# Performance work log

Measured on AMD Instinct MI355X. Metric: run time of the kernel, lower is better.

The kernel has to match this reference:

```python
import jax, jax.numpy as jnp
import numpy as np

N_X_AXIS = 128
N_Y_AXIS = 128
X_RANGE = (-2.0, 2.0)
Y_RANGE = (-2.0, 2.0)
BATCH = 4
N_CTX = 1024


def make_grid():
    # Give_2d_Grid: flattened (n_x*n_y, 2) grid, x-major (consistent with
    # the view(batch, n_x_axis, n_y_axis, 3) reshape in forward).
    gx = jnp.linspace(X_RANGE[0], X_RANGE[1], N_X_AXIS, dtype=jnp.float32)
    gy = jnp.linspace(Y_RANGE[0], Y_RANGE[1], N_Y_AXIS, dtype=jnp.float32)
    xx, yy = jnp.meshgrid(gx, gy, indexing='ij')  # (n_x, n_y)
    return jnp.stack([xx.ravel(), yy.ravel()], axis=-1)  # (n_x*n_y, 2)


def setup_inputs() -> dict:
    key = jax.random.key(0)
    k1, k2 = jax.random.split(key)
    X = jax.random.normal(k1, (BATCH, N_CTX, 2), dtype=jnp.float32)
    Y = jax.random.normal(k2, (BATCH, N_CTX, 2), dtype=jnp.float32)
    grid = make_grid()
    return {"X": X, "Y": Y, "grid": grid}


def reference(X, Y, grid):
    # RBF Gram matrix between grid points and context points X.
    # k(a,b) = exp(-||a-b||^2 / (2 l^2)), l = 1 (default length scale).
    # d2: (B, G, n)
    d2 = jnp.sum((grid[None, :, None, :] - X[:, None, :, :]) ** 2, axis=-1)
    Gram = jnp.exp(-0.5 * d2)  # (B, G, n)

    # Psi: prepend a column of ones -> (B, n, 3)
    ones = jnp.ones(Y.shape[:2] + (1,), dtype=Y.dtype)
    Expand_Y = jnp.concatenate([ones, Y], axis=-1)

    # Feature map: (B, G, 3)
    FM = jnp.einsum('bgn,bnc->bgc', Gram, Expand_Y)

    # Density-normalize the value channels by the density channel.
    density = FM[..., 0:1]
    FM = jnp.concatenate([density, FM[..., 1:] / density], axis=-1)

    # (B, G, 3) -> (B, n_x, n_y, 3) -> (B, 3, n_y, n_x)
    out = FM.reshape(X.shape[0], N_X_AXIS, N_Y_AXIS, 3)
    return out.transpose(0, 3, 2, 1)
```

## Files before the change

### kernel.cpp

```cpp
#include <hip/hip_runtime.h>


#define NCTX  1024
#define GPB   16384
#define OUTB  (3 * GPB)

typedef float f32x4  __attribute__((ext_vector_type(4)));
typedef short bf16x8 __attribute__((ext_vector_type(8)));

__device__ __forceinline__ float fast_exp2(float x) {
#if __has_builtin(__builtin_amdgcn_exp2f)
  return __builtin_amdgcn_exp2f(x);
#else
  return exp2f(x);
#endif
}

__device__ __forceinline__ unsigned short f2bf(float f) {
  union { float f; unsigned int u; } v; v.f = f;
  unsigned int r = v.u + 0x7FFFu + ((v.u >> 16) & 1u);
  return (unsigned short)(r >> 16);
}

__global__ __launch_bounds__(256) void tables_kernel(
    const float* __restrict__ X, const float* __restrict__ Y,
    const float* __restrict__ grid,
    unsigned short* __restrict__ A, unsigned short* __restrict__ Bt)
{
  const float SC = 0.84932180028801907f;
  const int blk = blockIdx.x;
  const int t   = threadIdx.x;
  const bool isA = blk < 512;
  const int r   = isA ? blk : blk - 512;
  const int b   = r >> 7;
  const int row = r & 127;
  const float gs = (isA ? grid[2 * row + 1]
                        : grid[2 * (row * 128)])
                   * SC;

  const float2* Xb = (const float2*)(X + b * NCTX * 2);
  const int n0 = 4 * t;

  if (isA) {
    const float2* Yb = (const float2*)(Y + b * NCTX * 2);
    ushort4 o0, o1, o2;
#pragma unroll
    for (int i = 0; i < 4; ++i) {
      float2 x = Xb[n0 + i];
      float2 y = Yb[n0 + i];
      float d  = gs - SC * x.y;
      float e  = fast_exp2(-(d * d));
      ((unsigned short*)&o0)[i] = f2bf(e);
      ((unsigned short*)&o1)[i] = f2bf(e * y.x);
      ((unsigned short*)&o2)[i] = f2bf(e * y.y);
    }
    unsigned short* a0 = A + (size_t)(b * 384 + row) * NCTX + n0;
    *(ushort4*)(a0)                 = o0;
    *(ushort4*)(a0 + 128 * NCTX)    = o1;
    *(ushort4*)(a0 + 256 * NCTX)    = o2;
  } else {
    ushort4 o;
#pragma unroll
    for (int i = 0; i < 4; ++i) {
      float2 x = Xb[n0 + i];
      float d  = gs - SC * x.x;
      ((unsigned short*)&o)[i] = f2bf(fast_exp2(-(d * d)));
    }
    *(ushort4*)(Bt + (size_t)(b * 128 + row) * NCTX + n0) = o;
  }
}

__global__ __launch_bounds__(64) void gemm_kernel(
    const unsigned short* __restrict__ A,
    const unsigned short* __restrict__ Bt,
    float* __restrict__ out)
{
  const int id   = blockIdx.x;
  const int b    = id / 192;
  const int rr   = id % 192;
  const int mt   = rr >> 3;
  const int nt   = rr & 7;
  const int lane = threadIdx.x;
  const int lo   = lane & 15;
  const int quad = lane >> 4;

  const bf16x8* ap = (const bf16x8*)(A  + (size_t)(b * 384 + mt * 16 + lo) * NCTX + quad * 8);
  const bf16x8* bp = (const bf16x8*)(Bt + (size_t)(b * 128 + nt * 16 + lo) * NCTX + quad * 8);

  f32x4 acc = {0.f, 0.f, 0.f, 0.f};
#pragma unroll 8
  for (int s = 0; s < 32; ++s) {
    bf16x8 av = ap[4 * s];
    bf16x8 bv = bp[4 * s];
    acc = __builtin_amdgcn_mfma_f32_16x16x32_bf16(av, bv, acc, 0, 0, 0);
  }

  float* ob = out + (size_t)b * OUTB + nt * 16 + lo;
  const int grow0 = mt * 16 + quad * 4;
#pragma unroll
  for (int g = 0; g < 4; ++g)
    ob[(size_t)(grow0 + g) * 128] = acc[g];
}

__global__ __launch_bounds__(256) void divide_kernel(float* __restrict__ out)
{
  const int id = blockIdx.x * 256 + threadIdx.x;
  const int b  = id >> 13;
  const int r  = id & 8191;
  const int c  = r >> 12;
  const int p4 = r & 4095;
  float4* base = (float4*)(out + (size_t)b * OUTB);
  float4 d = base[p4];
  float4* vp = base + (size_t)(c + 1) * 4096 + p4;
  float4 v = *vp;
  v.x /= d.x; v.y /= d.y; v.z /= d.z; v.w /= d.w;
  *vp = v;
}

extern "C" void kernel_launch(void* const* d_in, const int* in_sizes, int n_in,
                              void* d_out, int out_size, void* d_ws, size_t ws_size,
                              hipStream_t stream) {
  const float* X    = (const float*)d_in[0];
  const float* Y    = (const float*)d_in[1];
  const float* grid = (const float*)d_in[2];
  float* out        = (float*)d_out;

  unsigned short* A  = (unsigned short*)d_ws;
  unsigned short* Bt = A + (size_t)4 * 384 * NCTX;

  tables_kernel<<<dim3(1024), dim3(256), 0, stream>>>(X, Y, grid, A, Bt);
  gemm_kernel  <<<dim3(768),  dim3(64),  0, stream>>>(A, Bt, out);
  divide_kernel<<<dim3(128),  dim3(256), 0, stream>>>(out);
}
```

Measured before the change: 72.39 us.

## Fuse density division into GEMM by computing all three channels per block

The GEMM kernel now computes the density channel and both value channels for the same output tile in one block, reusing the loaded B fragment across three MFMAs. With all three accumulators in registers it divides the value channels by density in the epilogue, which removes the separate divide kernel launch and its global read-modify-write pass. The trade-off is fewer blocks (256 instead of 768) with more work each, which may lower occupancy and latency hiding on a GPU with many CUs.

Measured after the change: 71.58 us. Within noise of the previous version (-1.1%).

```diff
diff --git a/kernel.cpp b/kernel.cpp
--- a/kernel.cpp
+++ b/kernel.cpp
@@ -55,9 +55,9 @@
       ((unsigned short*)&o2)[i] = f2bf(e * y.y);
     }
     unsigned short* a0 = A + (size_t)(b * 384 + row) * NCTX + n0;
-    *(ushort4*)(a0)                 = o0;
-    *(ushort4*)(a0 + 128 * NCTX)    = o1;
-    *(ushort4*)(a0 + 256 * NCTX)    = o2;
+    *(ushort4*)(a0)              = o0;
+    *(ushort4*)(a0 + 128 * NCTX) = o1;
+    *(ushort4*)(a0 + 256 * NCTX) = o2;
   } else {
     ushort4 o;
 #pragma unroll
@@ -70,51 +70,44 @@
   }
 }
 
-__global__ __launch_bounds__(64) void gemm_kernel(
+__global__ __launch_bounds__(64) void gemm_div_kernel(
     const unsigned short* __restrict__ A,
     const unsigned short* __restrict__ Bt,
     float* __restrict__ out)
 {
   const int id   = blockIdx.x;
-  const int b    = id / 192;
-  const int rr   = id % 192;
-  const int mt   = rr >> 3;
-  const int nt   = rr & 7;
+  const int b    = id >> 6;
+  const int jyt  = (id >> 3) & 7;
+  const int ixt  = id & 7;
   const int lane = threadIdx.x;
   const int lo   = lane & 15;
   const int quad = lane >> 4;
 
-  const bf16x8* ap = (const bf16x8*)(A  + (size_t)(b * 384 + mt * 16 + lo) * NCTX + quad * 8);
-  const bf16x8* bp = (const bf16x8*)(Bt + (size_t)(b * 128 + nt * 16 + lo) * NCTX + quad * 8);
+  const size_t koff = (size_t)quad * 8;
+  const unsigned short* a0 = A  + ((size_t)(b * 384) + jyt * 16 + lo) * NCTX + koff;
+  const unsigned short* bp = Bt + ((size_t)(b * 128) + ixt * 16 + lo) * NCTX + koff;
 
-  f32x4 acc = {0.f, 0.f, 0.f, 0.f};
-#pragma unroll 8
+  f32x4 acc0 = {0.f,0.f,0.f,0.f}, acc1 = acc0, acc2 = acc0;
+#pragma unroll 4
   for (int s = 0; s < 32; ++s) {
-    bf16x8 av = ap[4 * s];
-    bf16x8 bv = bp[4 * s];
-    acc = __builtin_amdgcn_mfma_f32_16x16x32_bf16(av, bv, acc, 0, 0, 0);
+    const size_t o = (size_t)s * 32;
+    bf16x8 bv  = *(const bf16x8*)(bp + o);
+    bf16x8 a0v = *(const bf16x8*)(a0 + o);
+    bf16x8 a1v = *(const bf16x8*)(a0 + 128 * NCTX + o);
+    bf16x8 a2v = *(const bf16x8*)(a0 + 256 * NCTX + o);
+    acc0 = __builtin_amdgcn_mfma_f32_16x16x32_bf16(a0v, bv, acc0, 0, 0, 0);
+    acc1 = __builtin_amdgcn_mfma_f32_16x16x32_bf16(a1v, bv, acc1, 0, 0, 0);
+    acc2 = __builtin_amdgcn_mfma_f32_16x16x32_bf16(a2v, bv, acc2, 0, 0, 0);
   }
 
-  float* ob = out + (size_t)b * OUTB + nt * 16 + lo;
-  const int grow0 = mt * 16 + quad * 4;
+  float* ob = out + (size_t)b * OUTB + (jyt * 16 + quad * 4) * 128 + ixt * 16 + lo;
 #pragma unroll
-  for (int g = 0; g < 4; ++g)
-    ob[(size_t)(grow0 + g) * 128] = acc[g];
-}
-
-__global__ __launch_bounds__(256) void divide_kernel(float* __restrict__ out)
-{
-  const int id = blockIdx.x * 256 + threadIdx.x;
-  const int b  = id >> 13;
-  const int r  = id & 8191;
-  const int c  = r >> 12;
-  const int p4 = r & 4095;
-  float4* base = (float4*)(out + (size_t)b * OUTB);
-  float4 d = base[p4];
-  float4* vp = base + (size_t)(c + 1) * 4096 + p4;
-  float4 v = *vp;
-  v.x /= d.x; v.y /= d.y; v.z /= d.z; v.w /= d.w;
-  *vp = v;
+  for (int g = 0; g < 4; ++g) {
+    float d = acc0[g];
+    ob[(size_t)g * 128]               = d;
+    ob[(size_t)g * 128 + GPB]         = acc1[g] / d;
+    ob[(size_t)g * 128 + 2 * GPB]     = acc2[g] / d;
+  }
 }
 
 extern "C" void kernel_launch(void* const* d_in, const int* in_sizes, int n_in,
@@ -128,7 +121,6 @@
   unsigned short* A  = (unsigned short*)d_ws;
   unsigned short* Bt = A + (size_t)4 * 384 * NCTX;
 
-  tables_kernel<<<dim3(1024), dim3(256), 0, stream>>>(X, Y, grid, A, Bt);
-  gemm_kernel  <<<dim3(768),  dim3(64),  0, stream>>>(A, Bt, out);
-  divide_kernel<<<dim3(128),  dim3(256), 0, stream>>>(out);
+  tables_kernel  <<<dim3(1024), dim3(256), 0, stream>>>(X, Y, grid, A, Bt);
+  gemm_div_kernel<<<dim3(256),  dim3(64),  0, stream>>>(A, Bt, out);
 }
```
